# Optimization experiments

Measured on AMD Instinct MI355X. Metric: run time of the kernel, lower is better.

## Reference

```python
import jax, jax.numpy as jnp
import numpy as np

N_NODES = 50000
N_EDGES = 1600000
IN_CH = 512
OUT_CH = 64
ITERATIONS = 3


def _spmm(adj_index, adj_values, x):
    # sparse @ dense: out[r] = sum_{e: row[e]==r} vals[e] * x[col[e]]
    row, col = adj_index[0], adj_index[1]
    gathered = adj_values[:, None] * x[col]  # [E, F]
    return jax.ops.segment_sum(gathered, row, num_segments=x.shape[0])


def setup_inputs() -> dict:
    key = jax.random.key(0)
    k1, k2, k3, k4, k5 = jax.random.split(key, 5)
    adj_index = jax.random.randint(k1, (2, N_EDGES), 0, N_NODES, dtype=jnp.int64)
    # positive normalized-like edge weights ~ 1/avg_degree
    adj_values = jax.random.uniform(k2, (N_EDGES,), dtype=jnp.float32) / 32.0
    features = jax.random.normal(k3, (N_NODES, IN_CH), dtype=jnp.float32)
    xavier_w = float(np.sqrt(6.0 / (IN_CH + OUT_CH)))
    weight_matrix = jax.random.uniform(k4, (IN_CH, OUT_CH), dtype=jnp.float32, minval=-xavier_w, maxval=xavier_w)
    xavier_b = float(np.sqrt(6.0 / (1 + OUT_CH)))
    bias = jax.random.uniform(k5, (1, OUT_CH), dtype=jnp.float32, minval=-xavier_b, maxval=xavier_b)
    return {"adj_index": adj_index, "adj_values": adj_values, "features": features,
            "weight_matrix": weight_matrix, "bias": bias}


def reference(adj_index, adj_values, features, weight_matrix, bias):
    # dense projection (dropout_rate=0.0 / eval mode -> identity dropout)
    base = features @ weight_matrix  # [N, OUT_CH]
    # repeated sparse-dense propagation: A^(iterations-1) @ (X W)
    for _ in range(ITERATIONS - 1):
        base = _spmm(adj_index, adj_values, base)
    return base + bias
```

## Files before the change

### kernel.cpp

```cpp
#include <hip/hip_runtime.h>
#include <hip/hip_bf16.h>

typedef __attribute__((ext_vector_type(8))) __bf16 bf16x8;
typedef __attribute__((ext_vector_type(4))) float f32x4;

#define IN_CH 512
#define OUT_CH 64
#define BS 98
#define NB 512
#define CHUNK 8192
#define CAP 4096

__device__ inline unsigned short f2bf(float f) {
    __hip_bfloat16 h = __float2bfloat16(f);
    return __builtin_bit_cast(unsigned short, h);
}
__device__ inline float bf2f(unsigned short u) {
    return __uint_as_float(((unsigned)u) << 16);
}

__global__ __launch_bounds__(512) void prep_kernel(
    const float* __restrict__ W, __hip_bfloat16* __restrict__ Wf,
    int* __restrict__ bcur)
{
    const int t = blockIdx.x * 512 + threadIdx.x;
    if (t < NB) bcur[t] = t * CAP;
    const int ct = t >> 10;
    const int rem = t & 1023;
    const int ks = rem >> 6;
    const int l = rem & 63;
    const int col = ct * 16 + (l & 15);
    const int kb = ks * 32 + (l >> 4) * 8;
    __hip_bfloat16* dst = Wf + (size_t)t * 8;
    #pragma unroll
    for (int j = 0; j < 8; ++j)
        dst[j] = (__hip_bfloat16)W[(size_t)(kb + j) * OUT_CH + col];
}

__global__ __launch_bounds__(128) void gemm_kernel(
    const float* __restrict__ A, const bf16x8* __restrict__ wf,
    __hip_bfloat16* __restrict__ outb, int N)
{
    __shared__ __align__(16) char Abf[32 * 1024];

    const int tid = threadIdx.x;
    const int row0 = blockIdx.x * 32;

    float4 v[8], vn[8];
    #pragma unroll
    for (int j = 0; j < 8; ++j) {
        int f = j * 128 + tid;
        int row = f >> 7, c4 = f & 127;
        int rg = row0 + row; rg = rg < N ? rg : N - 1;
        v[j] = *(const float4*)(A + (size_t)rg * IN_CH + c4 * 4);
    }
    #pragma unroll 1
    for (int ob = 0; ob < 4; ++ob) {
        if (ob < 3) {
            #pragma unroll
            for (int j = 0; j < 8; ++j) {
                int f = ((ob + 1) * 8 + j) * 128 + tid;
                int row = f >> 7, c4 = f & 127;
                int rg = row0 + row; rg = rg < N ? rg : N - 1;
                vn[j] = *(const float4*)(A + (size_t)rg * IN_CH + c4 * 4);
            }
        }
        #pragma unroll
        for (int j = 0; j < 8; ++j) {
            int f = (ob * 8 + j) * 128 + tid;
            int row = f >> 7, c4 = f & 127;
            int blk = c4 >> 1, half = c4 & 1;
            ushort4 h;
            h.x = f2bf(v[j].x); h.y = f2bf(v[j].y);
            h.z = f2bf(v[j].z); h.w = f2bf(v[j].w);
            *(ushort4*)(Abf + row * 1024 + ((blk ^ (row & 7)) << 4) + (half << 3)) = h;
        }
        #pragma unroll
        for (int j = 0; j < 8; ++j) v[j] = vn[j];
    }
    __syncthreads();

    const int lane = tid & 63;
    const int wave = tid >> 6;
    const int arow = wave * 16 + (lane & 15);
    const int kgb = lane >> 4;

    bf16x8 a[16];
    #pragma unroll
    for (int ks = 0; ks < 16; ++ks)
        a[ks] = *(const bf16x8*)(Abf + arow * 1024 +
                                 (((ks * 4 + kgb) ^ (arow & 7)) << 4));

    const int colb = lane & 15;
    const int rr = row0 + wave * 16 + (lane >> 4) * 4;
    #pragma unroll 1
    for (int ct = 0; ct < 4; ++ct) {
        bf16x8 w[16];
        #pragma unroll
        for (int ks = 0; ks < 16; ++ks) w[ks] = wf[(ct * 16 + ks) * 64 + lane];
        f32x4 acc = {0.f, 0.f, 0.f, 0.f};
        #pragma unroll
        for (int ks = 0; ks < 16; ++ks)
            acc = __builtin_amdgcn_mfma_f32_16x16x32_bf16(a[ks], w[ks], acc, 0, 0, 0);
        int col = ct * 16 + colb;
        #pragma unroll
        for (int i = 0; i < 4; ++i) {
            int r = rr + i;
            if (r < N)
                outb[(size_t)r * OUT_CH + col] = __float2bfloat16(acc[i]);
        }
    }
}

__global__ __launch_bounds__(512) void bucket_scatter_kernel(
    const int* __restrict__ rows, const int* __restrict__ cols,
    const float* __restrict__ vals, int* __restrict__ bcur,
    int2* __restrict__ seg, int E)
{
    __shared__ int hist[NB];
    __shared__ int posBase[NB];
    const int tid = threadIdx.x;
    const int base = blockIdx.x * CHUNK + tid * 16;

    hist[tid] = 0;
    __syncthreads();

    int myb[16], mypack[16]; float myval[16];
    if (base + 16 <= E) {
        int4 r4[4], c4[4]; float4 v4[4];
        #pragma unroll
        for (int q = 0; q < 4; ++q) {
            r4[q] = *(const int4*)(rows + base + q * 4);
            c4[q] = *(const int4*)(cols + base + q * 4);
            v4[q] = *(const float4*)(vals + base + q * 4);
        }
        #pragma unroll
        for (int q = 0; q < 4; ++q) {
            int rr[4] = {r4[q].x, r4[q].y, r4[q].z, r4[q].w};
            int cc[4] = {c4[q].x, c4[q].y, c4[q].z, c4[q].w};
            float vv[4] = {v4[q].x, v4[q].y, v4[q].z, v4[q].w};
            #pragma unroll
            for (int u = 0; u < 4; ++u) {
                int j = q * 4 + u;
                int r = rr[u];
                int b = r / BS;
                myb[j] = b;
                mypack[j] = (cc[u] << 8) | (r - b * BS);
                myval[j] = vv[u];
                atomicAdd(&hist[b], 1);
            }
        }
    } else {
        #pragma unroll
        for (int j = 0; j < 16; ++j) {
            int e = base + j;
            myb[j] = -1;
            if (e < E) {
                int r = rows[e];
                int b = r / BS;
                myb[j] = b;
                mypack[j] = (cols[e] << 8) | (r - b * BS);
                myval[j] = vals[e];
                atomicAdd(&hist[b], 1);
            }
        }
    }
    __syncthreads();

    int h = hist[tid];
    if (h) posBase[tid] = atomicAdd(&bcur[tid], h);
    hist[tid] = 0;
    __syncthreads();

    #pragma unroll
    for (int j = 0; j < 16; ++j) {
        if (myb[j] >= 0) {
            int p = posBase[myb[j]] + atomicAdd(&hist[myb[j]], 1);
            int2 cv; cv.x = mypack[j]; cv.y = __float_as_int(myval[j]);
            seg[p] = cv;
        }
    }
}

__global__ __launch_bounds__(512) void sortspmm_kernel(
    const int* __restrict__ bcur, const int2* __restrict__ seg,
    unsigned* __restrict__ segc,
    int* __restrict__ offs, int* __restrict__ rend,
    const __hip_bfloat16* __restrict__ x,
    __hip_bfloat16* __restrict__ y1, int N)
{
    __shared__ unsigned sorted4[CAP];
    __shared__ int hist[BS + 1];
    __shared__ int cursor[BS];

    const int b = blockIdx.x;
    const int t = threadIdx.x;
    const int s = b * CAP;
    const int cnt = bcur[b] - s;

    if (t < BS + 1) hist[t] = 0;
    __syncthreads();

    int2 ed[8];
    #pragma unroll
    for (int j = 0; j < 8; ++j) {
        int idx = t + j * 512;
        if (idx < cnt) {
            ed[j] = seg[s + idx];
            atomicAdd(&hist[ed[j].x & 255], 1);
        }
    }
    __syncthreads();

    if (t == 0) {
        int run = 0;
        for (int i = 0; i < BS; ++i) { int c = hist[i]; hist[i] = run; run += c; }
        hist[BS] = run;
    }
    __syncthreads();

    if (t < BS) {
        cursor[t] = hist[t];
        offs[b * BS + t] = s + hist[t];
        rend[b * BS + t] = s + hist[t + 1];
    }
    __syncthreads();

    #pragma unroll
    for (int j = 0; j < 8; ++j) {
        int idx = t + j * 512;
        if (idx < cnt) {
            int pos = atomicAdd(&cursor[ed[j].x & 255], 1);
            unsigned col = ((unsigned)ed[j].x) >> 8;
            sorted4[pos] = (col << 16) | f2bf(__int_as_float(ed[j].y));
        }
    }
    __syncthreads();

    #pragma unroll
    for (int j = 0; j < 8; ++j) {
        int idx = t + j * 512;
        if (idx < cnt) segc[s + idx] = sorted4[idx];
    }

    const int lane = t & 63;
    const int wave = t >> 6;
    const int grp = lane >> 4;
    const int l16 = lane & 15;
    const ushort* xp = (const ushort*)x + l16 * 4;

    #pragma unroll 1
    for (int sweep = 0; sweep < 4; ++sweep) {
        int rr = sweep * 32 + wave * 4 + grp;
        int rrc = rr < BS ? rr : BS - 1;
        int rs = hist[rrc];
        int re = hist[rrc + 1];
        int gr = b * BS + rr;
        if (rr >= BS || gr >= N) re = rs;

        float4 acc = {0.f, 0.f, 0.f, 0.f};
        for (int i0 = rs; i0 < re; i0 += 16) {
            unsigned p[16];
            #pragma unroll
            for (int j = 0; j < 16; ++j) {
                int idx = i0 + j;
                p[j] = sorted4[idx < re ? idx : rs];
            }
            ushort4 xv[16];
            #pragma unroll
            for (int j = 0; j < 16; ++j)
                xv[j] = *(const ushort4*)(xp + (size_t)(p[j] >> 16) * OUT_CH);
            #pragma unroll
            for (int j = 0; j < 16; ++j) {
                float wv = (i0 + j < re) ? __uint_as_float(p[j] << 16) : 0.f;
                acc.x = fmaf(wv, bf2f(xv[j].x), acc.x);
                acc.y = fmaf(wv, bf2f(xv[j].y), acc.y);
                acc.z = fmaf(wv, bf2f(xv[j].z), acc.z);
                acc.w = fmaf(wv, bf2f(xv[j].w), acc.w);
            }
        }
        if (rr < BS && gr < N) {
            ushort4 h;
            h.x = f2bf(acc.x); h.y = f2bf(acc.y);
            h.z = f2bf(acc.z); h.w = f2bf(acc.w);
            *(ushort4*)((ushort*)y1 + (size_t)gr * OUT_CH + l16 * 4) = h;
        }
    }
}

__global__ __launch_bounds__(256) void spmm_row_kernel(
    const int* __restrict__ offs, const int* __restrict__ rend,
    const unsigned* __restrict__ segc,
    const __hip_bfloat16* __restrict__ x,
    float* __restrict__ yf, const float* __restrict__ bias, int N)
{
    const int tid = threadIdx.x;
    const int lane = tid & 63;
    const int wave = tid >> 6;
    const int grp = lane >> 4;
    const int l16 = lane & 15;

    int r = (blockIdx.x * 4 + wave) * 4 + grp;
    const bool rv = r < N;
    const int rc = rv ? r : N - 1;
    const int s = offs[rc];
    const int e = rv ? rend[rc] : s;

    int m = e - s;
    m = max(m, __shfl_xor(m, 16));
    m = max(m, __shfl_xor(m, 32));
    const int iters = (m + 15) >> 4;

    const ushort* xp = (const ushort*)x + l16 * 4;

    float4 acc = {0.f, 0.f, 0.f, 0.f};
    for (int it = 0; it < iters; ++it) {
        const int base = s + it * 16;
        unsigned p[16];
        #pragma unroll
        for (int j = 0; j < 16; ++j) {
            int idx = base + j;
            p[j] = segc[idx < e ? idx : s];
        }
        ushort4 xv[16];
        #pragma unroll
        for (int j = 0; j < 16; ++j)
            xv[j] = *(const ushort4*)(xp + (size_t)(p[j] >> 16) * OUT_CH);
        #pragma unroll
        for (int j = 0; j < 16; ++j) {
            int idx = base + j;
            float wv = (idx < e) ? __uint_as_float(p[j] << 16) : 0.f;
            acc.x = fmaf(wv, bf2f(xv[j].x), acc.x);
            acc.y = fmaf(wv, bf2f(xv[j].y), acc.y);
            acc.z = fmaf(wv, bf2f(xv[j].z), acc.z);
            acc.w = fmaf(wv, bf2f(xv[j].w), acc.w);
        }
    }

    if (rv) {
        float4 bv = *(const float4*)(bias + l16 * 4);
        float4 o;
        o.x = acc.x + bv.x; o.y = acc.y + bv.y;
        o.z = acc.z + bv.z; o.w = acc.w + bv.w;
        *(float4*)(yf + (size_t)r * OUT_CH + l16 * 4) = o;
    }
}

static inline size_t align_up(size_t v) { return (v + 255) & ~(size_t)255; }

extern "C" void kernel_launch(void* const* d_in, const int* in_sizes, int n_in,
                              void* d_out, int out_size, void* d_ws, size_t ws_size,
                              hipStream_t stream)
{
    const int*   adj  = (const int*)d_in[0];
    const float* vals = (const float*)d_in[1];
    const float* feat = (const float*)d_in[2];
    const float* Wm   = (const float*)d_in[3];
    const float* bias = (const float*)d_in[4];

    const int E = in_sizes[1];
    const int N = in_sizes[2] / IN_CH;
    const int* rows  = adj;
    const int* colsI = adj + E;

    char* w = (char*)d_ws;
    size_t o = 0;
    __hip_bfloat16* B0b = (__hip_bfloat16*)(w + o); o += align_up((size_t)N * OUT_CH * 2);
    __hip_bfloat16* Y1b = (__hip_bfloat16*)(w + o); o += align_up((size_t)N * OUT_CH * 2);
    __hip_bfloat16* Wf  = (__hip_bfloat16*)(w + o); o += align_up((size_t)IN_CH * OUT_CH * 2);
    int*      bcur = (int*)     (w + o); o += align_up(NB * sizeof(int));
    int*      offs = (int*)     (w + o); o += align_up((size_t)NB * BS * sizeof(int));
    int*      rend = (int*)     (w + o); o += align_up((size_t)NB * BS * sizeof(int));
    int2*     seg  = (int2*)    (w + o); o += align_up((size_t)NB * CAP * sizeof(int2));
    unsigned* segc = (unsigned*)(w + o); o += align_up((size_t)NB * CAP * sizeof(unsigned));
    (void)ws_size; (void)n_in; (void)out_size;

    prep_kernel<<<8, 512, 0, stream>>>(Wm, Wf, bcur);

    gemm_kernel<<<(N + 31) / 32, 128, 0, stream>>>(
        feat, (const bf16x8*)Wf, B0b, N);

    bucket_scatter_kernel<<<(E + CHUNK - 1) / CHUNK, 512, 0, stream>>>(
        rows, colsI, vals, bcur, seg, E);

    sortspmm_kernel<<<NB, 512, 0, stream>>>(
        bcur, seg, segc, offs, rend, B0b, Y1b, N);

    spmm_row_kernel<<<(N + 15) / 16, 256, 0, stream>>>(
        offs, rend, segc, Y1b, (float*)d_out, bias, N);
}
```

Before: 113.4 us.

## Stage bucket scatter in LDS and split edge records into packed word and row byte

```diff
diff --git a/kernel.cpp b/kernel.cpp
--- a/kernel.cpp
+++ b/kernel.cpp
@@ -115,18 +115,28 @@
 __global__ __launch_bounds__(512) void bucket_scatter_kernel(
     const int* __restrict__ rows, const int* __restrict__ cols,
     const float* __restrict__ vals, int* __restrict__ bcur,
-    int2* __restrict__ seg, int E)
-{
+    unsigned* __restrict__ segc, unsigned char* __restrict__ segr, int E)
+{
+    __shared__ unsigned      c_lds[CHUNK];
+    __shared__ unsigned char r_lds[CHUNK];
+    __shared__ unsigned short b_lds[CHUNK];
     __shared__ int hist[NB];
-    __shared__ int posBase[NB];
+    __shared__ int scn[NB];
+    __shared__ int lbase[NB];
+    __shared__ int runBase[NB];
+
     const int tid = threadIdx.x;
-    const int base = blockIdx.x * CHUNK + tid * 16;
+    const int c0 = blockIdx.x * CHUNK;
+    const int cnt = min(CHUNK, E - c0);
+    const int base = c0 + tid * 16;
 
     hist[tid] = 0;
     __syncthreads();
 
-    int myb[16], mypack[16]; float myval[16];
+    int myb[16]; unsigned myc[16]; unsigned char myr[16];
+    int nmine = 0;
     if (base + 16 <= E) {
+        nmine = 16;
         int4 r4[4], c4[4]; float4 v4[4];
         #pragma unroll
         for (int q = 0; q < 4; ++q) {
@@ -145,46 +155,66 @@
                 int r = rr[u];
                 int b = r / BS;
                 myb[j] = b;
-                mypack[j] = (cc[u] << 8) | (r - b * BS);
-                myval[j] = vv[u];
+                myr[j] = (unsigned char)(r - b * BS);
+                myc[j] = ((unsigned)cc[u] << 16) | f2bf(vv[u]);
                 atomicAdd(&hist[b], 1);
             }
         }
     } else {
-        #pragma unroll
+        #pragma unroll 1
         for (int j = 0; j < 16; ++j) {
             int e = base + j;
-            myb[j] = -1;
             if (e < E) {
                 int r = rows[e];
                 int b = r / BS;
                 myb[j] = b;
-                mypack[j] = (cols[e] << 8) | (r - b * BS);
-                myval[j] = vals[e];
+                myr[j] = (unsigned char)(r - b * BS);
+                myc[j] = ((unsigned)cols[e] << 16) | f2bf(vals[e]);
                 atomicAdd(&hist[b], 1);
+                nmine = j + 1;
             }
         }
     }
     __syncthreads();
 
-    int h = hist[tid];
-    if (h) posBase[tid] = atomicAdd(&bcur[tid], h);
-    hist[tid] = 0;
-    __syncthreads();
-
-    #pragma unroll
-    for (int j = 0; j < 16; ++j) {
-        if (myb[j] >= 0) {
-            int p = posBase[myb[j]] + atomicAdd(&hist[myb[j]], 1);
-            int2 cv; cv.x = mypack[j]; cv.y = __float_as_int(myval[j]);
-            seg[p] = cv;
-        }
+    {
+        int h = hist[tid];
+        scn[tid] = h;
+        __syncthreads();
+        for (int ofs = 1; ofs < NB; ofs <<= 1) {
+            int u = 0;
+            if (tid >= ofs) u = scn[tid - ofs];
+            __syncthreads();
+            if (tid >= ofs) scn[tid] += u;
+            __syncthreads();
+        }
+        int excl = scn[tid] - h;
+        lbase[tid] = excl;
+        hist[tid] = excl;
+        runBase[tid] = h ? atomicAdd(&bcur[tid], h) : 0;
+    }
+    __syncthreads();
+
+    #pragma unroll 1
+    for (int j = 0; j < nmine; ++j) {
+        int pos = atomicAdd(&hist[myb[j]], 1);
+        c_lds[pos] = myc[j];
+        r_lds[pos] = myr[j];
+        b_lds[pos] = (unsigned short)myb[j];
+    }
+    __syncthreads();
+
+    for (int idx = tid; idx < cnt; idx += 512) {
+        int b = b_lds[idx];
+        int gpos = runBase[b] + (idx - lbase[b]);
+        segc[gpos] = c_lds[idx];
+        segr[gpos] = r_lds[idx];
     }
 }
 
 __global__ __launch_bounds__(512) void sortspmm_kernel(
-    const int* __restrict__ bcur, const int2* __restrict__ seg,
-    unsigned* __restrict__ segc,
+    const int* __restrict__ bcur,
+    unsigned* __restrict__ segc, const unsigned char* __restrict__ segr,
     int* __restrict__ offs, int* __restrict__ rend,
     const __hip_bfloat16* __restrict__ x,
     __hip_bfloat16* __restrict__ y1, int N)
@@ -201,13 +231,14 @@
     if (t < BS + 1) hist[t] = 0;
     __syncthreads();
 
-    int2 ed[8];
+    unsigned ek[8]; unsigned char er[8];
     #pragma unroll
     for (int j = 0; j < 8; ++j) {
         int idx = t + j * 512;
         if (idx < cnt) {
-            ed[j] = seg[s + idx];
-            atomicAdd(&hist[ed[j].x & 255], 1);
+            ek[j] = segc[s + idx];
+            er[j] = segr[s + idx];
+            atomicAdd(&hist[er[j]], 1);
         }
     }
     __syncthreads();
@@ -230,9 +261,8 @@
     for (int j = 0; j < 8; ++j) {
         int idx = t + j * 512;
         if (idx < cnt) {
-            int pos = atomicAdd(&cursor[ed[j].x & 255], 1);
-            unsigned col = ((unsigned)ed[j].x) >> 8;
-            sorted4[pos] = (col << 16) | f2bf(__int_as_float(ed[j].y));
+            int pos = atomicAdd(&cursor[er[j]], 1);
+            sorted4[pos] = ek[j];
         }
     }
     __syncthreads();
@@ -368,11 +398,11 @@
     __hip_bfloat16* B0b = (__hip_bfloat16*)(w + o); o += align_up((size_t)N * OUT_CH * 2);
     __hip_bfloat16* Y1b = (__hip_bfloat16*)(w + o); o += align_up((size_t)N * OUT_CH * 2);
     __hip_bfloat16* Wf  = (__hip_bfloat16*)(w + o); o += align_up((size_t)IN_CH * OUT_CH * 2);
-    int*      bcur = (int*)     (w + o); o += align_up(NB * sizeof(int));
-    int*      offs = (int*)     (w + o); o += align_up((size_t)NB * BS * sizeof(int));
-    int*      rend = (int*)     (w + o); o += align_up((size_t)NB * BS * sizeof(int));
-    int2*     seg  = (int2*)    (w + o); o += align_up((size_t)NB * CAP * sizeof(int2));
-    unsigned* segc = (unsigned*)(w + o); o += align_up((size_t)NB * CAP * sizeof(unsigned));
+    int*           bcur = (int*)          (w + o); o += align_up(NB * sizeof(int));
+    int*           offs = (int*)          (w + o); o += align_up((size_t)NB * BS * sizeof(int));
+    int*           rend = (int*)          (w + o); o += align_up((size_t)NB * BS * sizeof(int));
+    unsigned*      segc = (unsigned*)     (w + o); o += align_up((size_t)NB * CAP * sizeof(unsigned));
+    unsigned char* segr = (unsigned char*)(w + o); o += align_up((size_t)NB * CAP);
     (void)ws_size; (void)n_in; (void)out_size;
 
     prep_kernel<<<8, 512, 0, stream>>>(Wm, Wf, bcur);
@@ -381,10 +411,10 @@
         feat, (const bf16x8*)Wf, B0b, N);
 
     bucket_scatter_kernel<<<(E + CHUNK - 1) / CHUNK, 512, 0, stream>>>(
-        rows, colsI, vals, bcur, seg, E);
+        rows, colsI, vals, bcur, segc, segr, E);
 
     sortspmm_kernel<<<NB, 512, 0, stream>>>(
-        bcur, seg, segc, offs, rend, B0b, Y1b, N);
+        bcur, segc, segr, offs, rend, B0b, Y1b, N);
 
     spmm_row_kernel<<<(N + 15) / 16, 256, 0, stream>>>(
         offs, rend, segc, Y1b, (float*)d_out, bias, N);
```

Result: no change. 113.4 us (-0.0%).
